# Kernel optimization log

Measured on AMD Instinct MI355X. Metric: run time of the kernel, lower is better.

Reference implementation:

```python
import jax, jax.numpy as jnp
import numpy as np

N_NODES = 50000
N_HYPEREDGES = 10000
NNZ = 800000


def setup_inputs() -> dict:
    key = jax.random.key(0)
    ks = jax.random.split(key, 8)
    x = jax.random.normal(ks[0], (N_NODES, 128), dtype=jnp.float32)
    edge = jax.random.randint(ks[1], (2, NNZ), 0, N_HYPEREDGES, dtype=jnp.int64)
    # Glorot-ish scaled weights per layer
    w1 = jax.random.normal(ks[2], (128, 128), dtype=jnp.float32) / np.sqrt(128)
    b1 = jnp.zeros((128,), dtype=jnp.float32)
    w2 = jax.random.normal(ks[3], (128, 64), dtype=jnp.float32) / np.sqrt(128)
    b2 = jnp.zeros((64,), dtype=jnp.float32)
    w3 = jax.random.normal(ks[4], (64, 32), dtype=jnp.float32) / np.sqrt(64)
    b3 = jnp.zeros((32,), dtype=jnp.float32)
    return {"x": x, "edge": edge, "w1": w1, "b1": b1, "w2": w2, "b2": b2, "w3": w3, "b3": b3}


def _hypergraph_conv(x, node_idx, edge_idx, w, b):
    """PyG HypergraphConv (no attention, unit hyperedge weights):
    X' = D^{-1} H B^{-1} H^T (X W + b)
    where H is the incidence matrix given by (node_idx, edge_idx) pairs,
    D = node degree, B = hyperedge degree.
    """
    xw = x @ w + b  # [N, F_out]
    ones = jnp.ones((node_idx.shape[0],), dtype=x.dtype)
    deg_e = jax.ops.segment_sum(ones, edge_idx, num_segments=N_HYPEREDGES)  # B
    deg_v = jax.ops.segment_sum(ones, node_idx, num_segments=N_NODES)      # D
    Binv = jnp.where(deg_e > 0, 1.0 / deg_e, 0.0)
    Dinv = jnp.where(deg_v > 0, 1.0 / deg_v, 0.0)
    # node -> hyperedge aggregation, normalized by hyperedge degree
    m_e = jax.ops.segment_sum(xw[node_idx], edge_idx, num_segments=N_HYPEREDGES) * Binv[:, None]
    # hyperedge -> node aggregation, normalized by node degree
    out = jax.ops.segment_sum(m_e[edge_idx], node_idx, num_segments=N_NODES) * Dinv[:, None]
    return out


def reference(x, edge, w1, b1, w2, b2, w3, b3):
    node_idx = edge[0]
    edge_idx = edge[1]
    h = jax.nn.relu(_hypergraph_conv(x, node_idx, edge_idx, w1, b1))
    h = jax.nn.relu(_hypergraph_conv(h, node_idx, edge_idx, w2, b2))
    h = jax.nn.relu(_hypergraph_conv(h, node_idx, edge_idx, w3, b3))
    return h
```

## Files before the change

### kernel.cpp

```cpp
#include <hip/hip_runtime.h>

#define N_NODES   50000
#define N_EDGES   10000
#define NNZ_TOT   800000
#define NACT      10000

#define SW   16
#define NB   625
#define CAP  1792

#define BW_IPT   32
#define BW_ITEMS (BW_IPT * 256)
#define BW_BLKS  ((NNZ_TOT + BW_ITEMS - 1) / BW_ITEMS)

#define G1_NRB   ((NACT + 31) / 32)
#define ZFB      96

__device__ __forceinline__ void bucket_write_body(
    const int* __restrict__ node_idx, const int* __restrict__ edge_idx,
    int* __restrict__ cntB, unsigned int* __restrict__ bktE,
    unsigned int* __restrict__ bktV, int nnz, int bwb)
{
    __shared__ int h[NB];
    const int tid  = threadIdx.x;
    const bool isV = bwb >= BW_BLKS;
    const int  blk = isV ? bwb - BW_BLKS : bwb;
    const int* keys = isV ? node_idx : edge_idx;
    const int* pays = isV ? edge_idx : node_idx;
    int* cnt = cntB + (isV ? NB : 0);
    unsigned int* bkt = isV ? bktV : bktE;

    for (int t = tid; t < NB; t += 256) h[t] = 0;
    __syncthreads();

    unsigned int pk[BW_IPT];
    const int base = blk * BW_ITEMS;
    #pragma unroll
    for (int j = 0; j < BW_IPT; ++j) {
        int k = base + j * 256 + tid;
        if (k < nnz) {
            unsigned int ky = (unsigned int)keys[k];
            unsigned int py = (unsigned int)pays[k];
            pk[j] = (ky << 16) | py;
            atomicAdd(&h[ky >> 4], 1);
        } else pk[j] = 0xFFFFFFFFu;
    }
    __syncthreads();
    for (int t = tid; t < NB; t += 256) {
        int c = h[t];
        h[t] = c ? atomicAdd(&cnt[t], c) : 0;
    }
    __syncthreads();
    #pragma unroll
    for (int j = 0; j < BW_IPT; ++j) {
        if (pk[j] != 0xFFFFFFFFu) {
            int b = (int)(pk[j] >> 20);
            int s = atomicAdd(&h[b], 1);
            if (s < CAP) bkt[(size_t)b * CAP + s] = pk[j];
        }
    }
}

template<int FIN, int FOUTT, int FB, int TM>
__device__ __forceinline__ void gemm_body(
    const float* __restrict__ X, const float* __restrict__ W,
    const float* __restrict__ Bias, float* __restrict__ Y,
    int nrows, int rb, int cb)
{
    constexpr int KB  = 32;
    constexpr int CGN = FB / 4;
    constexpr int RGN = 256 / CGN;
    constexpr int BM  = RGN * TM;
    static_assert(BM == 32, "BM must be 32");

    __shared__ float Xs[KB][BM + 4];
    __shared__ float Ws[KB][FB];

    const int tid  = threadIdx.x;
    const int cg   = tid % CGN;
    const int rg   = tid / CGN;
    const int row0 = rb * BM;
    const int col0 = cb * FB;

    float acc[TM][4];
    #pragma unroll
    for (int i = 0; i < TM; ++i)
        #pragma unroll
        for (int j = 0; j < 4; ++j) acc[i][j] = 0.f;

    for (int k0 = 0; k0 < FIN; k0 += KB) {
        {
            int r  = tid >> 3;
            int kq = tid & 7;
            int gr = row0 + r; if (gr >= nrows) gr = nrows - 1;
            float4 v = *(const float4*)&X[(size_t)gr * FIN + k0 + kq * 4];
            Xs[kq * 4 + 0][r] = v.x;
            Xs[kq * 4 + 1][r] = v.y;
            Xs[kq * 4 + 2][r] = v.z;
            Xs[kq * 4 + 3][r] = v.w;
        }
        constexpr int WIT = (KB * FB / 4) / 256;
        #pragma unroll
        for (int it = 0; it < WIT; ++it) {
            int idx = tid + it * 256;
            int k   = idx / (FB / 4);
            int cq  = idx % (FB / 4);
            *(float4*)&Ws[k][cq * 4] =
                *(const float4*)&W[(size_t)(k0 + k) * FOUTT + col0 + cq * 4];
        }
        __syncthreads();

        #pragma unroll 8
        for (int k = 0; k < KB; ++k) {
            float4 wv = *(const float4*)&Ws[k][cg * 4];
            float xr[TM];
            #pragma unroll
            for (int i = 0; i < TM; ++i) xr[i] = Xs[k][rg * TM + i];
            #pragma unroll
            for (int i = 0; i < TM; ++i) {
                acc[i][0] += xr[i] * wv.x;
                acc[i][1] += xr[i] * wv.y;
                acc[i][2] += xr[i] * wv.z;
                acc[i][3] += xr[i] * wv.w;
            }
        }
        __syncthreads();
    }

    float4 bv = *(const float4*)&Bias[col0 + cg * 4];
    #pragma unroll
    for (int i = 0; i < TM; ++i) {
        int gr = row0 + rg * TM + i;
        if (gr < nrows) {
            float4 o;
            o.x = acc[i][0] + bv.x; o.y = acc[i][1] + bv.y;
            o.z = acc[i][2] + bv.z; o.w = acc[i][3] + bv.w;
            *(float4*)&Y[(size_t)gr * FOUTT + col0 + cg * 4] = o;
        }
    }
}

__global__ __launch_bounds__(256) void build_gemm1_kernel(
    const int* __restrict__ node_idx, const int* __restrict__ edge_idx,
    int* __restrict__ cntB,
    unsigned int* __restrict__ bktE, unsigned int* __restrict__ bktV,
    const float* __restrict__ X, const float* __restrict__ W1,
    const float* __restrict__ B1, float* __restrict__ xw, int nnz)
{
    if (blockIdx.x < 2 * BW_BLKS) {
        bucket_write_body(node_idx, edge_idx, cntB, bktE, bktV, nnz, blockIdx.x);
    } else {
        int gb = blockIdx.x - 2 * BW_BLKS;
        gemm_body<128, 128, 64, 2>(X, W1, B1, xw, NACT, gb % G1_NRB, gb / G1_NRB);
    }
}

__global__ __launch_bounds__(256) void csr_finalize_kernel(
    const unsigned int* __restrict__ bktE, const unsigned int* __restrict__ bktV,
    const int* __restrict__ cntB,
    int2* __restrict__ segE, int2* __restrict__ segV,
    float* __restrict__ Binv, float* __restrict__ Dinv,
    int* __restrict__ csrE, int* __restrict__ csrV)
{
    __shared__ int cnt[SW];
    __shared__ int cur[SW];
    int b = blockIdx.x;
    const unsigned int* bkt; const int* cB; int2* seg; float* inv; int* csr;
    if (b < NB) { bkt = bktE; cB = cntB;      seg = segE; inv = Binv; csr = csrE; }
    else { b -= NB; bkt = bktV; cB = cntB + NB; seg = segV; inv = Dinv; csr = csrV; }
    const int lo = b * SW;
    const int p0 = b * CAP;
    int c_ = cB[b]; if (c_ > CAP) c_ = CAP;
    const int p1 = p0 + c_;

    if (threadIdx.x < SW) cnt[threadIdx.x] = 0;
    __syncthreads();
    for (int p = p0 + threadIdx.x; p < p1; p += 256) {
        int key = (int)(bkt[p] >> 16);
        atomicAdd(&cnt[key - lo], 1);
    }
    __syncthreads();
    if (threadIdx.x < 64) {
        int lane = threadIdx.x;
        int val = (lane < SW) ? cnt[lane] : 0;
        int x = val;
        #pragma unroll
        for (int d = 1; d < SW; d <<= 1) {
            int y = __shfl_up(x, d, 64);
            if (lane >= d) x += y;
        }
        if (lane < SW) {
            int beg = p0 + (x - val);
            int2 be; be.x = beg; be.y = beg + val;
            seg[lo + lane] = be;
            inv[lo + lane] = (val > 0) ? (1.0f / (float)val) : 0.0f;
            cur[lane]      = beg;
        }
    }
    __syncthreads();
    for (int p = p0 + threadIdx.x; p < p1; p += 256) {
        unsigned int pk = bkt[p];
        int key  = (int)(pk >> 16);
        int slot = atomicAdd(&cur[key - lo], 1);
        csr[slot] = (int)(pk & 0xFFFFu);
    }
}

template<int F, bool RELU>
__device__ __forceinline__ float4 seg_gather_acc(
    const float* __restrict__ SRC, const int2* __restrict__ seg,
    const int* __restrict__ lst, const float* __restrict__ inv,
    int s, int lane)
{
    constexpr int W = F / 4;
    constexpr int H = 64 / W;
    const int c = lane % W;
    const int h = lane / W;
    const int2 be = seg[s];
    const int start = be.x, end = be.y;
    const float* srcl = SRC + c * 4;
    float ax = 0.f, ay = 0.f, az = 0.f, aw = 0.f;
    int p = start + h;
    for (; p + 7 * H < end; p += 8 * H) {
        int r0 = lst[p],         r1 = lst[p + H],     r2 = lst[p + 2 * H], r3 = lst[p + 3 * H];
        int r4 = lst[p + 4 * H], r5 = lst[p + 5 * H], r6 = lst[p + 6 * H], r7 = lst[p + 7 * H];
        float4 a0 = *(const float4*)(srcl + (size_t)r0 * F);
        float4 a1 = *(const float4*)(srcl + (size_t)r1 * F);
        float4 a2 = *(const float4*)(srcl + (size_t)r2 * F);
        float4 a3 = *(const float4*)(srcl + (size_t)r3 * F);
        float4 a4 = *(const float4*)(srcl + (size_t)r4 * F);
        float4 a5 = *(const float4*)(srcl + (size_t)r5 * F);
        float4 a6 = *(const float4*)(srcl + (size_t)r6 * F);
        float4 a7 = *(const float4*)(srcl + (size_t)r7 * F);
        ax += (a0.x + a1.x) + (a2.x + a3.x) + (a4.x + a5.x) + (a6.x + a7.x);
        ay += (a0.y + a1.y) + (a2.y + a3.y) + (a4.y + a5.y) + (a6.y + a7.y);
        az += (a0.z + a1.z) + (a2.z + a3.z) + (a4.z + a5.z) + (a6.z + a7.z);
        aw += (a0.w + a1.w) + (a2.w + a3.w) + (a4.w + a5.w) + (a6.w + a7.w);
    }
    if (p + 3 * H < end) {
        int r0 = lst[p], r1 = lst[p + H], r2 = lst[p + 2 * H], r3 = lst[p + 3 * H];
        float4 a0 = *(const float4*)(srcl + (size_t)r0 * F);
        float4 a1 = *(const float4*)(srcl + (size_t)r1 * F);
        float4 a2 = *(const float4*)(srcl + (size_t)r2 * F);
        float4 a3 = *(const float4*)(srcl + (size_t)r3 * F);
        ax += (a0.x + a1.x) + (a2.x + a3.x);
        ay += (a0.y + a1.y) + (a2.y + a3.y);
        az += (a0.z + a1.z) + (a2.z + a3.z);
        aw += (a0.w + a1.w) + (a2.w + a3.w);
        p += 4 * H;
    }
    if (p + H < end) {
        int r0 = lst[p], r1 = lst[p + H];
        float4 a0 = *(const float4*)(srcl + (size_t)r0 * F);
        float4 a1 = *(const float4*)(srcl + (size_t)r1 * F);
        ax += a0.x + a1.x; ay += a0.y + a1.y;
        az += a0.z + a1.z; aw += a0.w + a1.w;
        p += 2 * H;
    }
    if (p < end) {
        int r = lst[p];
        float4 t = *(const float4*)(srcl + (size_t)r * F);
        ax += t.x; ay += t.y; az += t.z; aw += t.w;
    }
    #pragma unroll
    for (int d = W; d < 64; d <<= 1) {
        ax += __shfl_xor(ax, d);
        ay += __shfl_xor(ay, d);
        az += __shfl_xor(az, d);
        aw += __shfl_xor(aw, d);
    }
    float sc = inv[s];
    ax *= sc; ay *= sc; az *= sc; aw *= sc;
    if (RELU) {
        ax = fmaxf(ax, 0.f); ay = fmaxf(ay, 0.f);
        az = fmaxf(az, 0.f); aw = fmaxf(aw, 0.f);
    }
    float4 o; o.x = ax; o.y = ay; o.z = az; o.w = aw;
    return o;
}

template<int F, bool RELU>
__global__ __launch_bounds__(256) void seg_gather_s(
    const float* __restrict__ SRC, const int2* __restrict__ seg,
    const int* __restrict__ lst, const float* __restrict__ inv,
    float* __restrict__ DST, int nseg)
{
    int s = blockIdx.x * 4 + (threadIdx.x >> 6);
    s = __builtin_amdgcn_readfirstlane(s);
    if (s >= nseg) return;
    const int lane = threadIdx.x & 63;
    float4 o = seg_gather_acc<F, RELU>(SRC, seg, lst, inv, s, lane);
    if (lane < F / 4)
        *(float4*)(DST + (size_t)s * F + (lane % (F / 4)) * 4) = o;
}

template<int FIN, int FOUT>
__global__ __launch_bounds__(256) void seg_gather_gemm(
    const float* __restrict__ SRC, const int2* __restrict__ seg,
    const int* __restrict__ lst, const float* __restrict__ inv,
    const float* __restrict__ Wn, const float* __restrict__ Bn,
    float* __restrict__ OUT, int nseg)
{
    __shared__ float rowbuf[4][FIN];
    int s = blockIdx.x * 4 + (threadIdx.x >> 6);
    s = __builtin_amdgcn_readfirstlane(s);
    if (s >= nseg) return;
    const int lane = threadIdx.x & 63;
    const int w    = threadIdx.x >> 6;

    float4 o = seg_gather_acc<FIN, true>(SRC, seg, lst, inv, s, lane);
    if (lane < FIN / 4)
        *(float4*)&rowbuf[w][(lane % (FIN / 4)) * 4] = o;

    if (FOUT == 64) {
        const int j = lane;
        float acc = Bn[j];
        #pragma unroll 8
        for (int k = 0; k < FIN; ++k)
            acc += rowbuf[w][k] * Wn[(size_t)k * 64 + j];
        OUT[(size_t)s * 64 + j] = acc;
    } else {
        const int j = lane & 31;
        const int g = lane >> 5;
        float acc = 0.f;
        #pragma unroll 8
        for (int k = g * (FIN / 2); k < (g + 1) * (FIN / 2); ++k)
            acc += rowbuf[w][k] * Wn[(size_t)k * 32 + j];
        acc += __shfl_xor(acc, 32);
        if (lane < 32)
            OUT[(size_t)s * 32 + j] = acc + Bn[j];
    }
}

__global__ __launch_bounds__(256) void seg_gather_final(
    const float* __restrict__ SRC, const int2* __restrict__ seg,
    const int* __restrict__ lst, const float* __restrict__ inv,
    float* __restrict__ DST, int nsb)
{
    if ((int)blockIdx.x >= nsb) {
        const size_t total4 = (size_t)(N_NODES - NACT) * 32 / 4;
        float4* o4 = (float4*)(DST + (size_t)NACT * 32);
        float4 z; z.x = 0.f; z.y = 0.f; z.z = 0.f; z.w = 0.f;
        for (size_t i = (size_t)(blockIdx.x - nsb) * 256 + threadIdx.x;
             i < total4; i += (size_t)ZFB * 256)
            o4[i] = z;
        return;
    }
    int s = blockIdx.x * 4 + (threadIdx.x >> 6);
    s = __builtin_amdgcn_readfirstlane(s);
    if (s >= NACT) return;
    const int lane = threadIdx.x & 63;
    float4 o = seg_gather_acc<32, true>(SRC, seg, lst, inv, s, lane);
    if (lane < 8)
        *(float4*)(DST + (size_t)s * 32 + lane * 4) = o;
}

extern "C" void kernel_launch(void* const* d_in, const int* in_sizes, int n_in,
                              void* d_out, int out_size, void* d_ws, size_t ws_size,
                              hipStream_t stream)
{
    const float* x  = (const float*)d_in[0];
    const int* edge = (const int*)d_in[1];
    const float* w1 = (const float*)d_in[2];
    const float* b1 = (const float*)d_in[3];
    const float* w2 = (const float*)d_in[4];
    const float* b2 = (const float*)d_in[5];
    const float* w3 = (const float*)d_in[6];
    const float* b3 = (const float*)d_in[7];
    float* out = (float*)d_out;

    const int NNZ = NNZ_TOT;
    const int* node_idx = edge;
    const int* edge_idx = edge + NNZ;

    uintptr_t base = (uintptr_t)d_ws;
    size_t off = 0;
    auto take = [&](size_t nbytes) -> void* {
        off = (off + 255) & ~(size_t)255;
        void* p = (void*)(base + off);
        off += nbytes;
        return p;
    };
    int2*  segE  = (int2*) take((size_t)NACT * 8);
    int2*  segV  = (int2*) take((size_t)NACT * 8);
    float* Binv  = (float*)take((size_t)NACT * 4);
    float* Dinv  = (float*)take((size_t)NACT * 4);
    int*   cntB  = (int*)  take((size_t)2 * NB * 4);
    unsigned int* bktE = (unsigned int*)take((size_t)NB * CAP * 4);
    unsigned int* bktV = (unsigned int*)take((size_t)NB * CAP * 4);
    int*   csrE  = (int*)  take((size_t)NB * CAP * 4);
    int*   csrV  = (int*)  take((size_t)NB * CAP * 4);
    float* xw1   = (float*)take((size_t)NACT * 128 * 4);
    float* xw2   = (float*)take((size_t)NACT * 64 * 4);
    float* xw3   = (float*)take((size_t)NACT * 32 * 4);
    float* me    = (float*)take((size_t)NACT * 128 * 4);

    hipMemsetAsync(cntB, 0, (size_t)2 * NB * 4, stream);

    build_gemm1_kernel<<<2 * BW_BLKS + G1_NRB * 2, 256, 0, stream>>>(
        node_idx, edge_idx, cntB, bktE, bktV, x, w1, b1, xw1, NNZ);
    csr_finalize_kernel<<<2 * NB, 256, 0, stream>>>(
        bktE, bktV, cntB, segE, segV, Binv, Dinv, csrE, csrV);

    const int nsbA = (NACT + 3) / 4;

    seg_gather_s<128, false><<<nsbA, 256, 0, stream>>>(xw1, segE, csrE, Binv, me, NACT);
    seg_gather_gemm<128, 64><<<nsbA, 256, 0, stream>>>(
        me, segV, csrV, Dinv, w2, b2, xw2, NACT);

    seg_gather_s<64, false><<<nsbA, 256, 0, stream>>>(xw2, segE, csrE, Binv, me, NACT);
    seg_gather_gemm<64, 32><<<nsbA, 256, 0, stream>>>(
        me, segV, csrV, Dinv, w3, b3, xw3, NACT);

    seg_gather_s<32, false><<<nsbA, 256, 0, stream>>>(xw3, segE, csrE, Binv, me, NACT);
    seg_gather_final<<<nsbA + ZFB, 256, 0, stream>>>(me, segV, csrV, Dinv, out, nsbA);
}
```

Measured before the change: 221.5 us.

## Store intermediate feature buffers in fp16 to halve gather traffic

Changes the xw1/xw2/xw3 and message buffers from fp32 to fp16. Producers convert their outputs to half, and every gather loop loads 8 halves per 16-byte load and accumulates in fp32. This roughly halves the bytes moved in the random-row gathers, which likely dominate the runtime. It costs extra rounding error from fp16 storage of the intermediates, and each lane now covers 8 columns instead of 4, so there are more shuffle reductions.

```diff
diff --git a/kernel.cpp b/kernel.cpp
--- a/kernel.cpp
+++ b/kernel.cpp
@@ -1,4 +1,5 @@
 #include <hip/hip_runtime.h>
+#include <hip/hip_fp16.h>
 
 #define N_NODES   50000
 #define N_EDGES   10000
@@ -15,6 +16,7 @@
 
 #define G1_NRB   ((NACT + 31) / 32)
 #define ZFB      96
+
 
 __device__ __forceinline__ void bucket_write_body(
     const int* __restrict__ node_idx, const int* __restrict__ edge_idx,
@@ -64,7 +66,7 @@
 template<int FIN, int FOUTT, int FB, int TM>
 __device__ __forceinline__ void gemm_body(
     const float* __restrict__ X, const float* __restrict__ W,
-    const float* __restrict__ Bias, float* __restrict__ Y,
+    const float* __restrict__ Bias, __half* __restrict__ Y,
     int nrows, int rb, int cb)
 {
     constexpr int KB  = 32;
@@ -132,10 +134,9 @@
     for (int i = 0; i < TM; ++i) {
         int gr = row0 + rg * TM + i;
         if (gr < nrows) {
-            float4 o;
-            o.x = acc[i][0] + bv.x; o.y = acc[i][1] + bv.y;
-            o.z = acc[i][2] + bv.z; o.w = acc[i][3] + bv.w;
-            *(float4*)&Y[(size_t)gr * FOUTT + col0 + cg * 4] = o;
+            __half2* yp = (__half2*)&Y[(size_t)gr * FOUTT + col0 + cg * 4];
+            yp[0] = __floats2half2_rn(acc[i][0] + bv.x, acc[i][1] + bv.y);
+            yp[1] = __floats2half2_rn(acc[i][2] + bv.z, acc[i][3] + bv.w);
         }
     }
 }
@@ -145,7 +146,7 @@
     int* __restrict__ cntB,
     unsigned int* __restrict__ bktE, unsigned int* __restrict__ bktV,
     const float* __restrict__ X, const float* __restrict__ W1,
-    const float* __restrict__ B1, float* __restrict__ xw, int nnz)
+    const float* __restrict__ B1, __half* __restrict__ xw, int nnz)
 {
     if (blockIdx.x < 2 * BW_BLKS) {
         bucket_write_body(node_idx, edge_idx, cntB, bktE, bktV, nnz, blockIdx.x);
@@ -206,100 +207,108 @@
     }
 }
 
+__device__ __forceinline__ void acc8(float a[8], const float4& t)
+{
+    const __half2* hp = reinterpret_cast<const __half2*>(&t);
+    #pragma unroll
+    for (int j = 0; j < 4; ++j) {
+        float2 f = __half22float2(hp[j]);
+        a[2 * j]     += f.x;
+        a[2 * j + 1] += f.y;
+    }
+}
+
 template<int F, bool RELU>
-__device__ __forceinline__ float4 seg_gather_acc(
-    const float* __restrict__ SRC, const int2* __restrict__ seg,
+__device__ __forceinline__ void seg_gather_acc_h(
+    const __half* __restrict__ SRC, const int2* __restrict__ seg,
     const int* __restrict__ lst, const float* __restrict__ inv,
-    int s, int lane)
-{
-    constexpr int W = F / 4;
+    int s, int lane, float a[8])
+{
+    constexpr int W = F / 8;
     constexpr int H = 64 / W;
     const int c = lane % W;
     const int h = lane / W;
     const int2 be = seg[s];
     const int start = be.x, end = be.y;
-    const float* srcl = SRC + c * 4;
-    float ax = 0.f, ay = 0.f, az = 0.f, aw = 0.f;
+    const __half* srcl = SRC + c * 8;
+    #pragma unroll
+    for (int j = 0; j < 8; ++j) a[j] = 0.f;
+
     int p = start + h;
     for (; p + 7 * H < end; p += 8 * H) {
         int r0 = lst[p],         r1 = lst[p + H],     r2 = lst[p + 2 * H], r3 = lst[p + 3 * H];
         int r4 = lst[p + 4 * H], r5 = lst[p + 5 * H], r6 = lst[p + 6 * H], r7 = lst[p + 7 * H];
-        float4 a0 = *(const float4*)(srcl + (size_t)r0 * F);
-        float4 a1 = *(const float4*)(srcl + (size_t)r1 * F);
-        float4 a2 = *(const float4*)(srcl + (size_t)r2 * F);
-        float4 a3 = *(const float4*)(srcl + (size_t)r3 * F);
-        float4 a4 = *(const float4*)(srcl + (size_t)r4 * F);
-        float4 a5 = *(const float4*)(srcl + (size_t)r5 * F);
-        float4 a6 = *(const float4*)(srcl + (size_t)r6 * F);
-        float4 a7 = *(const float4*)(srcl + (size_t)r7 * F);
-        ax += (a0.x + a1.x) + (a2.x + a3.x) + (a4.x + a5.x) + (a6.x + a7.x);
-        ay += (a0.y + a1.y) + (a2.y + a3.y) + (a4.y + a5.y) + (a6.y + a7.y);
-        az += (a0.z + a1.z) + (a2.z + a3.z) + (a4.z + a5.z) + (a6.z + a7.z);
-        aw += (a0.w + a1.w) + (a2.w + a3.w) + (a4.w + a5.w) + (a6.w + a7.w);
+        float4 t0 = *(const float4*)(srcl + (size_t)r0 * F);
+        float4 t1 = *(const float4*)(srcl + (size_t)r1 * F);
+        float4 t2 = *(const float4*)(srcl + (size_t)r2 * F);
+        float4 t3 = *(const float4*)(srcl + (size_t)r3 * F);
+        float4 t4 = *(const float4*)(srcl + (size_t)r4 * F);
+        float4 t5 = *(const float4*)(srcl + (size_t)r5 * F);
+        float4 t6 = *(const float4*)(srcl + (size_t)r6 * F);
+        float4 t7 = *(const float4*)(srcl + (size_t)r7 * F);
+        acc8(a, t0); acc8(a, t1); acc8(a, t2); acc8(a, t3);
+        acc8(a, t4); acc8(a, t5); acc8(a, t6); acc8(a, t7);
     }
     if (p + 3 * H < end) {
         int r0 = lst[p], r1 = lst[p + H], r2 = lst[p + 2 * H], r3 = lst[p + 3 * H];
-        float4 a0 = *(const float4*)(srcl + (size_t)r0 * F);
-        float4 a1 = *(const float4*)(srcl + (size_t)r1 * F);
-        float4 a2 = *(const float4*)(srcl + (size_t)r2 * F);
-        float4 a3 = *(const float4*)(srcl + (size_t)r3 * F);
-        ax += (a0.x + a1.x) + (a2.x + a3.x);
-        ay += (a0.y + a1.y) + (a2.y + a3.y);
-        az += (a0.z + a1.z) + (a2.z + a3.z);
-        aw += (a0.w + a1.w) + (a2.w + a3.w);
+        float4 t0 = *(const float4*)(srcl + (size_t)r0 * F);
+        float4 t1 = *(const float4*)(srcl + (size_t)r1 * F);
+        float4 t2 = *(const float4*)(srcl + (size_t)r2 * F);
+        float4 t3 = *(const float4*)(srcl + (size_t)r3 * F);
+        acc8(a, t0); acc8(a, t1); acc8(a, t2); acc8(a, t3);
         p += 4 * H;
     }
     if (p + H < end) {
         int r0 = lst[p], r1 = lst[p + H];
-        float4 a0 = *(const float4*)(srcl + (size_t)r0 * F);
-        float4 a1 = *(const float4*)(srcl + (size_t)r1 * F);
-        ax += a0.x + a1.x; ay += a0.y + a1.y;
-        az += a0.z + a1.z; aw += a0.w + a1.w;
+        float4 t0 = *(const float4*)(srcl + (size_t)r0 * F);
+        float4 t1 = *(const float4*)(srcl + (size_t)r1 * F);
+        acc8(a, t0); acc8(a, t1);
         p += 2 * H;
     }
     if (p < end) {
         int r = lst[p];
         float4 t = *(const float4*)(srcl + (size_t)r * F);
-        ax += t.x; ay += t.y; az += t.z; aw += t.w;
+        acc8(a, t);
     }
     #pragma unroll
     for (int d = W; d < 64; d <<= 1) {
-        ax += __shfl_xor(ax, d);
-        ay += __shfl_xor(ay, d);
-        az += __shfl_xor(az, d);
-        aw += __shfl_xor(aw, d);
+        #pragma unroll
+        for (int j = 0; j < 8; ++j) a[j] += __shfl_xor(a[j], d);
     }
     float sc = inv[s];
-    ax *= sc; ay *= sc; az *= sc; aw *= sc;
-    if (RELU) {
-        ax = fmaxf(ax, 0.f); ay = fmaxf(ay, 0.f);
-        az = fmaxf(az, 0.f); aw = fmaxf(aw, 0.f);
-    }
-    float4 o; o.x = ax; o.y = ay; o.z = az; o.w = aw;
-    return o;
+    #pragma unroll
+    for (int j = 0; j < 8; ++j) {
+        a[j] *= sc;
+        if (RELU) a[j] = fmaxf(a[j], 0.f);
+    }
 }
 
 template<int F, bool RELU>
-__global__ __launch_bounds__(256) void seg_gather_s(
-    const float* __restrict__ SRC, const int2* __restrict__ seg,
+__global__ __launch_bounds__(256) void seg_gather_s_h(
+    const __half* __restrict__ SRC, const int2* __restrict__ seg,
     const int* __restrict__ lst, const float* __restrict__ inv,
-    float* __restrict__ DST, int nseg)
+    __half* __restrict__ DST, int nseg)
 {
     int s = blockIdx.x * 4 + (threadIdx.x >> 6);
     s = __builtin_amdgcn_readfirstlane(s);
     if (s >= nseg) return;
     const int lane = threadIdx.x & 63;
-    float4 o = seg_gather_acc<F, RELU>(SRC, seg, lst, inv, s, lane);
-    if (lane < F / 4)
-        *(float4*)(DST + (size_t)s * F + (lane % (F / 4)) * 4) = o;
+    float a[8];
+    seg_gather_acc_h<F, RELU>(SRC, seg, lst, inv, s, lane, a);
+    if (lane < F / 8) {
+        alignas(16) __half2 hh[4];
+        #pragma unroll
+        for (int j = 0; j < 4; ++j) hh[j] = __floats2half2_rn(a[2 * j], a[2 * j + 1]);
+        *(float4*)(DST + (size_t)s * F + lane * 8) = *reinterpret_cast<float4*>(hh);
+    }
 }
 
 template<int FIN, int FOUT>
-__global__ __launch_bounds__(256) void seg_gather_gemm(
-    const float* __restrict__ SRC, const int2* __restrict__ seg,
+__global__ __launch_bounds__(256) void seg_gather_gemm_h(
+    const __half* __restrict__ SRC, const int2* __restrict__ seg,
     const int* __restrict__ lst, const float* __restrict__ inv,
     const float* __restrict__ Wn, const float* __restrict__ Bn,
-    float* __restrict__ OUT, int nseg)
+    __half* __restrict__ OUT, int nseg)
 {
     __shared__ float rowbuf[4][FIN];
     int s = blockIdx.x * 4 + (threadIdx.x >> 6);
@@ -308,9 +317,12 @@
     const int lane = threadIdx.x & 63;
     const int w    = threadIdx.x >> 6;
 
-    float4 o = seg_gather_acc<FIN, true>(SRC, seg, lst, inv, s, lane);
-    if (lane < FIN / 4)
-        *(float4*)&rowbuf[w][(lane % (FIN / 4)) * 4] = o;
+    float a[8];
+    seg_gather_acc_h<FIN, true>(SRC, seg, lst, inv, s, lane, a);
+    if (lane < FIN / 8) {
+        *(float4*)&rowbuf[w][lane * 8]     = make_float4(a[0], a[1], a[2], a[3]);
+        *(float4*)&rowbuf[w][lane * 8 + 4] = make_float4(a[4], a[5], a[6], a[7]);
+    }
 
     if (FOUT == 64) {
         const int j = lane;
@@ -318,7 +330,7 @@
         #pragma unroll 8
         for (int k = 0; k < FIN; ++k)
             acc += rowbuf[w][k] * Wn[(size_t)k * 64 + j];
-        OUT[(size_t)s * 64 + j] = acc;
+        OUT[(size_t)s * 64 + j] = __float2half_rn(acc);
     } else {
         const int j = lane & 31;
         const int g = lane >> 5;
@@ -328,12 +340,12 @@
             acc += rowbuf[w][k] * Wn[(size_t)k * 32 + j];
         acc += __shfl_xor(acc, 32);
         if (lane < 32)
-            OUT[(size_t)s * 32 + j] = acc + Bn[j];
-    }
-}
-
-__global__ __launch_bounds__(256) void seg_gather_final(
-    const float* __restrict__ SRC, const int2* __restrict__ seg,
+            OUT[(size_t)s * 32 + j] = __float2half_rn(acc + Bn[j]);
+    }
+}
+
+__global__ __launch_bounds__(256) void seg_gather_final_h(
+    const __half* __restrict__ SRC, const int2* __restrict__ seg,
     const int* __restrict__ lst, const float* __restrict__ inv,
     float* __restrict__ DST, int nsb)
 {
@@ -350,9 +362,12 @@
     s = __builtin_amdgcn_readfirstlane(s);
     if (s >= NACT) return;
     const int lane = threadIdx.x & 63;
-    float4 o = seg_gather_acc<32, true>(SRC, seg, lst, inv, s, lane);
-    if (lane < 8)
-        *(float4*)(DST + (size_t)s * 32 + lane * 4) = o;
+    float a[8];
+    seg_gather_acc_h<32, true>(SRC, seg, lst, inv, s, lane, a);
+    if (lane < 4) {
+        *(float4*)(DST + (size_t)s * 32 + lane * 8)     = make_float4(a[0], a[1], a[2], a[3]);
+        *(float4*)(DST + (size_t)s * 32 + lane * 8 + 4) = make_float4(a[4], a[5], a[6], a[7]);
+    }
 }
 
 extern "C" void kernel_launch(void* const* d_in, const int* in_sizes, int n_in,
@@ -390,10 +405,10 @@
     unsigned int* bktV = (unsigned int*)take((size_t)NB * CAP * 4);
     int*   csrE  = (int*)  take((size_t)NB * CAP * 4);
     int*   csrV  = (int*)  take((size_t)NB * CAP * 4);
-    float* xw1   = (float*)take((size_t)NACT * 128 * 4);
-    float* xw2   = (float*)take((size_t)NACT * 64 * 4);
-    float* xw3   = (float*)take((size_t)NACT * 32 * 4);
-    float* me    = (float*)take((size_t)NACT * 128 * 4);
+    __half* xw1  = (__half*)take((size_t)NACT * 128 * 2);
+    __half* xw2  = (__half*)take((size_t)NACT * 64 * 2);
+    __half* xw3  = (__half*)take((size_t)NACT * 32 * 2);
+    __half* me   = (__half*)take((size_t)NACT * 128 * 2);
 
     hipMemsetAsync(cntB, 0, (size_t)2 * NB * 4, stream);
 
@@ -404,14 +419,14 @@
 
     const int nsbA = (NACT + 3) / 4;
 
-    seg_gather_s<128, false><<<nsbA, 256, 0, stream>>>(xw1, segE, csrE, Binv, me, NACT);
-    seg_gather_gemm<128, 64><<<nsbA, 256, 0, stream>>>(
+    seg_gather_s_h<128, false><<<nsbA, 256, 0, stream>>>(xw1, segE, csrE, Binv, me, NACT);
+    seg_gather_gemm_h<128, 64><<<nsbA, 256, 0, stream>>>(
         me, segV, csrV, Dinv, w2, b2, xw2, NACT);
 
-    seg_gather_s<64, false><<<nsbA, 256, 0, stream>>>(xw2, segE, csrE, Binv, me, NACT);
-    seg_gather_gemm<64, 32><<<nsbA, 256, 0, stream>>>(
+    seg_gather_s_h<64, false><<<nsbA, 256, 0, stream>>>(xw2, segE, csrE, Binv, me, NACT);
+    seg_gather_gemm_h<64, 32><<<nsbA, 256, 0, stream>>>(
         me, segV, csrV, Dinv, w3, b3, xw3, NACT);
 
-    seg_gather_s<32, false><<<nsbA, 256, 0, stream>>>(xw3, segE, csrE, Binv, me, NACT);
-    seg_gather_final<<<nsbA + ZFB, 256, 0, stream>>>(me, segV, csrV, Dinv, out, nsbA);
-}
+    seg_gather_s_h<32, false><<<nsbA, 256, 0, stream>>>(xw3, segE, csrE, Binv, me, NACT);
+    seg_gather_final_h<<<nsbA + ZFB, 256, 0, stream>>>(me, segV, csrV, Dinv, out, nsbA);
+}
```

Result: faster. 192.0 us (-13.3%).
